# Kernel optimization log

Measured on AMD Instinct MI355X. Metric: run time of the kernel, lower is better.

The kernel has to match this reference:

```python
import jax, jax.numpy as jnp
import numpy as np

BN_EPS = 1e-5


def three_nn(unknown, known):
    # squared pairwise distances via gemm form: ||u||^2 + ||k||^2 - 2 u.k
    # unknown: (B, n, 3), known: (B, m, 3) -> d: (B, n, m)
    u2 = jnp.sum(unknown * unknown, axis=-1, keepdims=True)          # (B, n, 1)
    k2 = jnp.sum(known * known, axis=-1)[:, None, :]                 # (B, 1, m)
    d = u2 + k2 - 2.0 * jnp.einsum('bnc,bmc->bnm', unknown, known)   # (B, n, m)
    neg_d, idx = jax.lax.top_k(-d, 3)                                # 3 smallest
    return -neg_d, idx                                               # (B,n,3), (B,n,3) int32


def three_interpolate(known_feats, idx, weight):
    # known_feats: (B, C, m), idx/weight: (B, n, 3) -> (B, C, n)
    g = jnp.take_along_axis(known_feats[:, :, None, :], idx[:, None, :, :], axis=3)  # (B,C,n,3)
    return jnp.sum(g * weight[:, None, :, :], axis=3)


def conv1x1(x, W, b):
    # x: (B, C_in, N), W: (C_out, C_in), b: (C_out,)
    return jnp.einsum('oc,bcn->bon', W, x) + b[None, :, None]


def batchnorm(x, gamma, beta):
    # training-mode BN over (B, N) per channel, biased variance
    mean = jnp.mean(x, axis=(0, 2), keepdims=True)
    var = jnp.mean((x - mean) ** 2, axis=(0, 2), keepdims=True)
    xn = (x - mean) * jax.lax.rsqrt(var + BN_EPS)
    return xn * gamma[None, :, None] + beta[None, :, None]


def setup_inputs() -> dict:
    key = jax.random.key(0)
    ks = jax.random.split(key, 16)
    B, n, m = 16, 4096, 1024
    C1, C2, C = 128, 256, 256  # in_channels, known feat channels (=mlp[0]), mlp width
    inp = {
        'unknown': jax.random.normal(ks[0], (B, n, 3), jnp.float32),
        'known': jax.random.normal(ks[1], (B, m, 3), jnp.float32),
        'unknow_feats': jax.random.normal(ks[2], (B, C1, n), jnp.float32),
        'known_feats': jax.random.normal(ks[3], (B, C2, m), jnp.float32),
        # mlp_unknow: Conv1d(C1->C) + BN (no relu)
        'Wu': jax.random.normal(ks[4], (C, C1), jnp.float32) * (1.0 / np.sqrt(C1)),
        'bu': jnp.zeros((C,), jnp.float32),
        'gu': jnp.ones((C,), jnp.float32),
        'betau': jnp.zeros((C,), jnp.float32),
        # mlp_convs[0]: Conv1d(C->C) + BN + relu
        'W1': jax.random.normal(ks[5], (C, C), jnp.float32) * (1.0 / np.sqrt(C)),
        'b1': jnp.zeros((C,), jnp.float32),
        'g1': jnp.ones((C,), jnp.float32),
        'beta1': jnp.zeros((C,), jnp.float32),
        # mlp_convs[1]: Conv1d(C->C) + BN + relu
        'W2': jax.random.normal(ks[6], (C, C), jnp.float32) * (1.0 / np.sqrt(C)),
        'b2': jnp.zeros((C,), jnp.float32),
        'g2': jnp.ones((C,), jnp.float32),
        'beta2': jnp.zeros((C,), jnp.float32),
    }
    return inp


def reference(unknown, known, unknow_feats, known_feats,
              Wu, bu, gu, betau, W1, b1, g1, beta1, W2, b2, g2, beta2):
    dist, idx = three_nn(unknown, known)            # squared dists (B,n,3)
    dist_recip = 1.0 / (dist + 1e-8)
    norm = jnp.sum(dist_recip, axis=2, keepdims=True)
    weight = dist_recip / norm
    interpolated = three_interpolate(known_feats, idx, weight)   # (B, 256, n)

    skip = batchnorm(conv1x1(unknow_feats, Wu, bu), gu, betau)   # (B, 256, n)
    x = interpolated + skip
    x = jax.nn.relu(batchnorm(conv1x1(x, W1, b1), g1, beta1))
    x = jax.nn.relu(batchnorm(conv1x1(x, W2, b2), g2, beta2))
    return x
```

## Files before the change

kernel.cpp:

```cpp
#include <hip/hip_runtime.h>
#include <hip/hip_bf16.h>
#include <cstddef>
#include <cstdint>

#define BATCH 16
#define NPTS  4096
#define MPTS  1024
#define PTOT  65536
#define C1    128
#define C2    256

typedef short bf16x8 __attribute__((ext_vector_type(8)));
typedef float f32x4  __attribute__((ext_vector_type(4)));
typedef unsigned int u32x4 __attribute__((ext_vector_type(4)));

static __device__ __forceinline__ float bf2f(unsigned int u16) {
    union { unsigned int i; float f; } v; v.i = u16 << 16; return v.f;
}
static __device__ __forceinline__ unsigned short f2bf(float f) {
    union { float f; unsigned int i; } v; v.f = f;
    unsigned int u = v.i;
    return (unsigned short)((u + 0x7FFFu + ((u >> 16) & 1u)) >> 16);
}

static __device__ __forceinline__ void st_wt_b128(void* p, u32x4 v) {
    asm volatile("global_store_dwordx4 %0, %1, off sc0 sc1" :: "v"(p), "v"(v) : "memory");
}
static __device__ __forceinline__ void st_wt_f128(void* p, f32x4 v) {
    asm volatile("global_store_dwordx4 %0, %1, off sc0 sc1" :: "v"(p), "v"(v) : "memory");
}
static __device__ __forceinline__ void st_wt_b32(void* p, unsigned v) {
    asm volatile("global_store_dword %0, %1, off sc0 sc1" :: "v"(p), "v"(v) : "memory");
}
static __device__ __forceinline__ void st_wt_b16(void* p, unsigned v) {
    asm volatile("global_store_short %0, %1, off sc0 sc1" :: "v"(p), "v"(v) : "memory");
}

template <int SWZ>
__global__ void k_transpose(const float* __restrict__ in, unsigned short* __restrict__ out,
                            int C, int N) {
    __shared__ float tile[64][65];
    int b  = blockIdx.z;
    int n0 = blockIdx.x * 64;
    int c0 = blockIdx.y * 64;
    const float* src = in + (size_t)b * C * N;
    unsigned short* dst = out + (size_t)b * N * C;
    int t  = threadIdx.x;
    int t4 = t >> 6;
    int tn = t & 63;
#pragma unroll
    for (int i = 0; i < 16; ++i) {
        int cc = i * 4 + t4;
        tile[cc][tn] = src[(size_t)(c0 + cc) * N + n0 + tn];
    }
    __syncthreads();
#pragma unroll
    for (int i = 0; i < 16; ++i) {
        int nn = i * 4 + t4;
        int p  = n0 + nn;
        int c  = c0 + tn;
        size_t off;
        if (SWZ) off = (size_t)p * C + (size_t)((((c >> 3) ^ (p & 7)) << 3) + (c & 7));
        else     off = (size_t)p * C + c;
        st_wt_b16(dst + off, (unsigned)f2bf(tile[tn][nn]));
    }
}

__global__ void k_cvt_pack(const float* __restrict__ in, unsigned short* __restrict__ out, int K) {
    int tid = blockIdx.x * 256 + threadIdx.x;
    if (tid >= 256 * K) return;
    int ch = tid / K, k = tid % K;
    int ks = k >> 5, lhi = (k >> 3) & 3, e = k & 7;
    int wv = ch >> 6, i = (ch >> 4) & 3, llo = ch & 15;
    int lane = lhi * 16 + llo;
    st_wt_b16(out + ((size_t)((ks * 16 + wv * 4 + i) * 64 + lane)) * 8 + e,
              (unsigned)f2bf(in[tid]));
}

static __device__ __forceinline__ bool nn_less(float da, int ia, float db, int ib) {
    return (da < db) || (da == db && ia < ib);
}

__global__ void k_three_nn(const float* __restrict__ unknown, const float* __restrict__ known,
                           int* __restrict__ idx_out, float* __restrict__ w_out) {
    __shared__ float4 kpt[MPTS + 4];
    int t  = threadIdx.x;
    int p0 = blockIdx.x * 64;
    int b  = p0 >> 12;
    const float* kb = known + (size_t)b * MPTS * 3;
    for (int i = t; i < MPTS; i += 256) {
        float x = kb[i * 3 + 0], y = kb[i * 3 + 1], z = kb[i * 3 + 2];
        float dd = __fadd_rn(__fadd_rn(__fmul_rn(x, x), __fmul_rn(y, y)), __fmul_rn(z, z));
        float4 v; v.x = x; v.y = y; v.z = z; v.w = dd;
        kpt[i + (i >> 8)] = v;
    }
    __syncthreads();

    int q = t & 3;
    int p = p0 + (t >> 2);
    const float* up = unknown + (size_t)p * 3;
    float ux = up[0], uy = up[1], uz = up[2];
    float u2 = __fadd_rn(__fadd_rn(__fmul_rn(ux, ux), __fmul_rn(uy, uy)), __fmul_rn(uz, uz));

    float d0 = INFINITY, d1 = INFINITY, d2 = INFINITY;
    int   i0 = 0, i1 = 0, i2 = 0;
    int base = q * 257;
#pragma unroll 4
    for (int it = 0; it < 256; ++it) {
        float4 kp = kpt[base + it];
        float dot = __fadd_rn(__fadd_rn(__fmul_rn(ux, kp.x), __fmul_rn(uy, kp.y)),
                              __fmul_rn(uz, kp.z));
        float d = __fsub_rn(__fadd_rn(u2, kp.w), __fmul_rn(2.0f, dot));
        int k = q * 256 + it;
        if (d < d0)      { d2 = d1; i2 = i1; d1 = d0; i1 = i0; d0 = d; i0 = k; }
        else if (d < d1) { d2 = d1; i2 = i1; d1 = d;  i1 = k; }
        else if (d < d2) { d2 = d;  i2 = k; }
    }

#pragma unroll
    for (int m = 1; m <= 2; m <<= 1) {
        float e0 = __shfl_xor(d0, m, 64), e1 = __shfl_xor(d1, m, 64), e2 = __shfl_xor(d2, m, 64);
        int   j0 = __shfl_xor(i0, m, 64), j1 = __shfl_xor(i1, m, 64), j2 = __shfl_xor(i2, m, 64);
        float a0 = d0, a1 = d1, a2 = d2; int x0 = i0, x1 = i1, x2 = i2;
        float b0 = e0, b1 = e1, b2 = e2; int y0 = j0, y1 = j1, y2 = j2;
        bool tk = nn_less(a0, x0, b0, y0);
        d0 = tk ? a0 : b0; i0 = tk ? x0 : y0;
        float na0 = tk ? a1 : a0; int nx0 = tk ? x1 : x0;
        float na1 = tk ? a2 : a1; int nx1 = tk ? x2 : x1;
        float nb0 = tk ? b0 : b1; int ny0 = tk ? y0 : y1;
        float nb1 = tk ? b1 : b2; int ny1 = tk ? y1 : y2;
        tk = nn_less(na0, nx0, nb0, ny0);
        d1 = tk ? na0 : nb0; i1 = tk ? nx0 : ny0;
        float ma0 = tk ? na1 : na0; int mx0 = tk ? nx1 : nx0;
        float mb0 = tk ? nb0 : nb1; int my0 = tk ? ny0 : ny1;
        tk = nn_less(ma0, mx0, mb0, my0);
        d2 = tk ? ma0 : mb0; i2 = tk ? mx0 : my0;
    }

    if (q == 0) {
        float r0 = 1.0f / (d0 + 1e-8f), r1 = 1.0f / (d1 + 1e-8f), r2 = 1.0f / (d2 + 1e-8f);
        float norm = r0 + r1 + r2;
        size_t pg = (size_t)p;
        st_wt_b32(idx_out + pg * 3 + 0, (unsigned)i0);
        st_wt_b32(idx_out + pg * 3 + 1, (unsigned)i1);
        st_wt_b32(idx_out + pg * 3 + 2, (unsigned)i2);
        union { float f; unsigned u; } w0v, w1v, w2v;
        w0v.f = r0 / norm; w1v.f = r1 / norm; w2v.f = r2 / norm;
        st_wt_b32(w_out + pg * 3 + 0, w0v.u);
        st_wt_b32(w_out + pg * 3 + 1, w1v.u);
        st_wt_b32(w_out + pg * 3 + 2, w2v.u);
    }
}

template <int K, int MODE>
__global__ void k_gemm(
        const unsigned short* __restrict__ Wp,
        const unsigned short* __restrict__ X,
        const float* __restrict__ Xf,
        const float* __restrict__ bias,
        const float* __restrict__ aff_a,
        const float* __restrict__ aff_c,
        unsigned short* __restrict__ Y,
        float* __restrict__ partial) {
    constexpr int NK = K / 32;
    constexpr int TILE_BYTES = 64 * K * 2;
    constexpr int SMEM_BYTES = TILE_BYTES > 32768 ? TILE_BYTES : 32768;
    __shared__ char smem[SMEM_BYTES];

    const int t    = threadIdx.x;
    const int p0   = blockIdx.x * 64;
    const int wv   = t >> 6;
    const int lane = t & 63;
    const int lhi  = lane >> 4, llo = lane & 15;

    if (MODE == 0) {
        const char* src = (const char*)(X + (size_t)p0 * K);
        constexpr int ITERS = TILE_BYTES / (256 * 16);
#pragma unroll
        for (int i = 0; i < ITERS; ++i) {
            int off = (i * 256 + t) * 16;
            __builtin_amdgcn_global_load_lds(
                (const __attribute__((address_space(1))) unsigned int*)(src + off),
                (__attribute__((address_space(3))) unsigned int*)(smem + off),
                16, 0, 0);
        }
    } else if (MODE == 1) {
        constexpr int CPR = K / 8;
#pragma unroll
        for (int i = 0; i < (64 * CPR) / 256; ++i) {
            int f   = i * 256 + t;
            int row = f / CPR, qp = f % CPR;
            int col = qp ^ (row & 7);
            uint4 v = *(const uint4*)(X + (size_t)(p0 + row) * K + qp * 8);
            unsigned int w[4] = {v.x, v.y, v.z, v.w};
            float4 a0 = *(const float4*)(aff_a + col * 8);
            float4 a1 = *(const float4*)(aff_a + col * 8 + 4);
            float4 cc0 = *(const float4*)(aff_c + col * 8);
            float4 cc1 = *(const float4*)(aff_c + col * 8 + 4);
            float aa[8] = {a0.x, a0.y, a0.z, a0.w, a1.x, a1.y, a1.z, a1.w};
            float cc[8] = {cc0.x, cc0.y, cc0.z, cc0.w, cc1.x, cc1.y, cc1.z, cc1.w};
#pragma unroll
            for (int q2 = 0; q2 < 4; ++q2) {
                float lo = fmaxf(bf2f(w[q2] & 0xffff) * aa[q2 * 2]     + cc[q2 * 2],     0.0f);
                float hi = fmaxf(bf2f(w[q2] >> 16)    * aa[q2 * 2 + 1] + cc[q2 * 2 + 1], 0.0f);
                w[q2] = (unsigned int)f2bf(lo) | ((unsigned int)f2bf(hi) << 16);
            }
            uint4 o; o.x = w[0]; o.y = w[1]; o.z = w[2]; o.w = w[3];
            *(uint4*)(smem + row * (K * 2) + qp * 16) = o;
        }
    } else {
        int c  = t >> 1;
        int ph = (t & 1) * 32;
        int b  = p0 >> 12;
        const float* src = Xf + ((size_t)b * C1 + c) * NPTS + (p0 & 4095) + ph;
#pragma unroll
        for (int k = 0; k < 8; ++k) {
            float4 v = *(const float4*)(src + k * 4);
#pragma unroll
            for (int e = 0; e < 4; ++e) {
                int p = ph + k * 4 + e;
                float f = (e == 0) ? v.x : (e == 1) ? v.y : (e == 2) ? v.z : v.w;
                *(unsigned short*)(smem + p * (K * 2) + ((((c >> 3) ^ (p & 7)) << 4) + (c & 7) * 2))
                    = f2bf(f);
            }
        }
    }

    const unsigned short* wbase = Wp + ((size_t)(wv * 256) + lane) * 8;
    bf16x8 wA[4], wB[4];
#pragma unroll
    for (int i = 0; i < 4; ++i)
        wA[i] = *(const bf16x8*)(wbase + i * 512);

    __syncthreads();

    f32x4 acc[4][4];
#pragma unroll
    for (int i = 0; i < 4; ++i)
#pragma unroll
        for (int j = 0; j < 4; ++j) acc[i][j] = (f32x4){0.f, 0.f, 0.f, 0.f};

#pragma unroll
    for (int ks = 0; ks < NK; ks += 2) {
#pragma unroll
        for (int i = 0; i < 4; ++i)
            wB[i] = *(const bf16x8*)(wbase + (size_t)(ks + 1) * 8192 + i * 512);
        {
            bf16x8 bb[4];
#pragma unroll
            for (int j = 0; j < 4; ++j) {
                int row = j * 16 + llo;
                int cp  = (ks * 4 + lhi) ^ (row & 7);
                bb[j] = *(const bf16x8*)(smem + row * (K * 2) + cp * 16);
            }
#pragma unroll
            for (int i = 0; i < 4; ++i)
#pragma unroll
                for (int j = 0; j < 4; ++j)
                    acc[i][j] = __builtin_amdgcn_mfma_f32_16x16x32_bf16(wA[i], bb[j], acc[i][j], 0, 0, 0);
        }
        if (ks + 2 < NK) {
#pragma unroll
            for (int i = 0; i < 4; ++i)
                wA[i] = *(const bf16x8*)(wbase + (size_t)(ks + 2) * 8192 + i * 512);
        }
        {
            bf16x8 bb[4];
#pragma unroll
            for (int j = 0; j < 4; ++j) {
                int row = j * 16 + llo;
                int cp  = ((ks + 1) * 4 + lhi) ^ (row & 7);
                bb[j] = *(const bf16x8*)(smem + row * (K * 2) + cp * 16);
            }
#pragma unroll
            for (int i = 0; i < 4; ++i)
#pragma unroll
                for (int j = 0; j < 4; ++j)
                    acc[i][j] = __builtin_amdgcn_mfma_f32_16x16x32_bf16(wB[i], bb[j], acc[i][j], 0, 0, 0);
        }
    }

    __syncthreads();
#pragma unroll
    for (int i = 0; i < 4; ++i) {
        int cbase = wv * 64 + i * 16 + lhi * 4;
        float4 bv = *(const float4*)(bias + cbase);
        int c8 = cbase >> 3, hf = lhi & 1;
        float s0 = 0.f, s1 = 0.f, s2 = 0.f, s3 = 0.f;
        float q0 = 0.f, q1 = 0.f, q2 = 0.f, q3 = 0.f;
#pragma unroll
        for (int j = 0; j < 4; ++j) {
            int row = j * 16 + llo;
            float y0 = acc[i][j][0] + bv.x;
            float y1 = acc[i][j][1] + bv.y;
            float y2 = acc[i][j][2] + bv.z;
            float y3 = acc[i][j][3] + bv.w;
            s0 += y0; q0 += y0 * y0;  s1 += y1; q1 += y1 * y1;
            s2 += y2; q2 += y2 * y2;  s3 += y3; q3 += y3 * y3;
            unsigned int lo = (unsigned int)f2bf(y0) | ((unsigned int)f2bf(y1) << 16);
            unsigned int hi = (unsigned int)f2bf(y2) | ((unsigned int)f2bf(y3) << 16);
            uint2 o; o.x = lo; o.y = hi;
            *(uint2*)(smem + row * 512 + ((c8 ^ (row & 7)) << 4) + hf * 8) = o;
        }
#pragma unroll
        for (int m = 1; m <= 8; m <<= 1) {
            s0 += __shfl_xor(s0, m, 64); q0 += __shfl_xor(q0, m, 64);
            s1 += __shfl_xor(s1, m, 64); q1 += __shfl_xor(q1, m, 64);
            s2 += __shfl_xor(s2, m, 64); q2 += __shfl_xor(q2, m, 64);
            s3 += __shfl_xor(s3, m, 64); q3 += __shfl_xor(q3, m, 64);
        }
        if (llo == 0) {
            f32x4 sv = {s0, s1, s2, s3};
            f32x4 qv = {q0, q1, q2, q3};
            st_wt_f128(partial + (size_t)blockIdx.x * 512 + cbase, sv);
            st_wt_f128(partial + (size_t)blockIdx.x * 512 + 256 + cbase, qv);
        }
    }
    __syncthreads();
    {
        const char* ysrc = smem + wv * 8192 + lane * 16;
        char* ydst = (char*)(Y + (size_t)p0 * 256) + wv * 8192 + lane * 16;
#pragma unroll
        for (int i2 = 0; i2 < 8; ++i2) {
            u32x4 v = *(const u32x4*)(ysrc + i2 * 1024);
            st_wt_b128(ydst + i2 * 1024, v);
        }
    }
}

__global__ void k_red1(const float* __restrict__ partial, float* __restrict__ partA) {
    int t = threadIdx.x, g = blockIdx.x;
    float s = 0.f, q = 0.f;
#pragma unroll
    for (int i = 0; i < 16; ++i) {
        const float* pp = partial + (size_t)(g * 16 + i) * 512;
        s += pp[t]; q += pp[256 + t];
    }
    union { float f; unsigned u; } sv, qv; sv.f = s; qv.f = q;
    st_wt_b32(partA + g * 512 + t, sv.u);
    st_wt_b32(partA + g * 512 + 256 + t, qv.u);
}

__global__ void k_finalize(const float* __restrict__ partA, const float* __restrict__ gamma,
                           const float* __restrict__ beta, float* __restrict__ aff_a,
                           float* __restrict__ aff_c) {
    int c = threadIdx.x;
    float s = 0.f, q = 0.f;
#pragma unroll 8
    for (int i = 0; i < 64; ++i) { s += partA[i * 512 + c]; q += partA[i * 512 + 256 + c]; }
    float mean = s * (1.0f / PTOT);
    float var  = fmaxf(q * (1.0f / PTOT) - mean * mean, 0.0f);
    float a    = gamma[c] / sqrtf(var + 1e-5f);
    union { float f; unsigned u; } av, cv;
    av.f = a; cv.f = beta[c] - mean * a;
    st_wt_b32(aff_a + c, av.u);
    st_wt_b32(aff_c + c, cv.u);
}

__global__ void k_build_x(const unsigned short* __restrict__ y0, const unsigned short* __restrict__ kfT,
                          const int* __restrict__ idx, const float* __restrict__ wgt,
                          const float* __restrict__ aff_a, const float* __restrict__ aff_c,
                          unsigned short* __restrict__ X) {
    int t   = threadIdx.x;
    int p   = blockIdx.x * 8 + (t >> 5);
    int col = t & 31;
    int c0  = col * 8;
    int b   = p >> 12;
    int pos = col ^ (p & 7);
    int i0 = idx[p * 3 + 0], i1 = idx[p * 3 + 1], i2 = idx[p * 3 + 2];
    float w0 = wgt[p * 3 + 0], w1 = wgt[p * 3 + 1], w2 = wgt[p * 3 + 2];
    const size_t kb = (size_t)b * MPTS * C2;
    uint4 v0 = *(const uint4*)(kfT + kb + (size_t)i0 * C2 + c0);
    uint4 v1 = *(const uint4*)(kfT + kb + (size_t)i1 * C2 + c0);
    uint4 v2 = *(const uint4*)(kfT + kb + (size_t)i2 * C2 + c0);
    uint4 vy = *(const uint4*)(y0 + (size_t)p * C2 + pos * 8);
    const unsigned int* u0 = (const unsigned int*)&v0;
    const unsigned int* u1 = (const unsigned int*)&v1;
    const unsigned int* u2 = (const unsigned int*)&v2;
    const unsigned int* uy = (const unsigned int*)&vy;
    unsigned int r[4];
#pragma unroll
    for (int q = 0; q < 4; ++q) {
        int c = c0 + q * 2;
        float lo = w0 * bf2f(u0[q] & 0xffff) + w1 * bf2f(u1[q] & 0xffff) + w2 * bf2f(u2[q] & 0xffff)
                 + bf2f(uy[q] & 0xffff) * aff_a[c] + aff_c[c];
        float hi = w0 * bf2f(u0[q] >> 16) + w1 * bf2f(u1[q] >> 16) + w2 * bf2f(u2[q] >> 16)
                 + bf2f(uy[q] >> 16) * aff_a[c + 1] + aff_c[c + 1];
        r[q] = (unsigned int)f2bf(lo) | ((unsigned int)f2bf(hi) << 16);
    }
    u32x4 vout; vout.x = r[0]; vout.y = r[1]; vout.z = r[2]; vout.w = r[3];
    st_wt_b128(X + (size_t)p * C2 + pos * 8, vout);
}

__global__ void k_final(const unsigned short* __restrict__ Y2, const float* __restrict__ aff_a,
                        const float* __restrict__ aff_c, float* __restrict__ out) {
    __shared__ float tile[64][65];
    int p0 = blockIdx.x * 64;
    int c0 = blockIdx.y * 64;
    int t  = threadIdx.x;
    int t4 = t >> 6, t64 = t & 63;
#pragma unroll
    for (int i = 0; i < 16; ++i) {
        int r = i * 4 + t4;
        int p = p0 + r;
        int c = c0 + t64;
        float v = bf2f(Y2[(size_t)p * 256 + (((c >> 3) ^ (p & 7)) << 3) + (c & 7)])
                  * aff_a[c] + aff_c[c];
        tile[t64][r] = fmaxf(v, 0.0f);
    }
    __syncthreads();
    int b   = p0 >> 12;
    int pin = p0 & 4095;
#pragma unroll
    for (int i = 0; i < 16; ++i) {
        int cc = i * 4 + t4;
        __builtin_nontemporal_store(tile[cc][t64],
            out + ((size_t)b * 256 + c0 + cc) * 4096 + pin + t64);
    }
}

extern "C" void kernel_launch(void* const* d_in, const int* in_sizes, int n_in,
                              void* d_out, int out_size, void* d_ws, size_t ws_size,
                              hipStream_t stream) {
    const float* unknown = (const float*)d_in[0];
    const float* known   = (const float*)d_in[1];
    const float* ufeat   = (const float*)d_in[2];
    const float* kfeat   = (const float*)d_in[3];
    const float* Wu      = (const float*)d_in[4];
    const float* bu      = (const float*)d_in[5];
    const float* gu      = (const float*)d_in[6];
    const float* betau   = (const float*)d_in[7];
    const float* W1      = (const float*)d_in[8];
    const float* b1      = (const float*)d_in[9];
    const float* g1      = (const float*)d_in[10];
    const float* beta1   = (const float*)d_in[11];
    const float* W2      = (const float*)d_in[12];
    const float* b2      = (const float*)d_in[13];
    const float* g2      = (const float*)d_in[14];
    const float* beta2   = (const float*)d_in[15];
    float* out = (float*)d_out;

    char* ws = (char*)d_ws;
    unsigned short* reg0 = (unsigned short*)ws;
    unsigned short* ybuf = (unsigned short*)(ws + ((size_t)32 << 20));
    unsigned short* kfT  = (unsigned short*)(ws + ((size_t)64 << 20));
    unsigned short* Wub  = (unsigned short*)(ws + ((size_t)72 << 20));
    unsigned short* W1b  = Wub + 256 * 128;
    unsigned short* W2b  = W1b + 256 * 256;
    int*   idxb = (int*)(W2b + 256 * 256);
    float* wgtb = (float*)(idxb + (size_t)PTOT * 3);
    float* affa0 = wgtb + (size_t)PTOT * 3;
    float* affc0 = affa0 + 256;
    float* affa1 = affc0 + 256;
    float* affc1 = affa1 + 256;
    float* affa2 = affc1 + 256;
    float* affc2 = affa2 + 256;
    float* part0  = (float*)(ws + ((size_t)16 << 20));
    float* partA0 = (float*)(ws + ((size_t)18 << 20));
    float* part12  = (float*)(ws + ((size_t)64 << 20));
    float* partA12 = (float*)(ws + ((size_t)66 << 20));
    if (ws_size < ((size_t)75 << 20)) return;

    k_transpose<0><<<dim3(MPTS / 64, C2 / 64, BATCH), 256, 0, stream>>>(kfeat, kfT, C2, MPTS);
    k_cvt_pack<<<128, 256, 0, stream>>>(Wu, Wub, 128);
    k_cvt_pack<<<256, 256, 0, stream>>>(W1, W1b, 256);
    k_cvt_pack<<<256, 256, 0, stream>>>(W2, W2b, 256);

    k_three_nn<<<PTOT / 64, 256, 0, stream>>>(unknown, known, idxb, wgtb);

    k_gemm<C1, 2><<<PTOT / 64, 256, 0, stream>>>(Wub, nullptr, ufeat, bu, nullptr, nullptr,
                                                 ybuf, part0);
    k_red1<<<64, 256, 0, stream>>>(part0, partA0);
    k_finalize<<<1, 256, 0, stream>>>(partA0, gu, betau, affa0, affc0);

    k_build_x<<<PTOT / 8, 256, 0, stream>>>(ybuf, kfT, idxb, wgtb, affa0, affc0, reg0);

    k_gemm<C2, 0><<<PTOT / 64, 256, 0, stream>>>(W1b, reg0, nullptr, b1, nullptr, nullptr,
                                                 ybuf, part12);
    k_red1<<<64, 256, 0, stream>>>(part12, partA12);
    k_finalize<<<1, 256, 0, stream>>>(partA12, g1, beta1, affa1, affc1);

    k_gemm<C2, 1><<<PTOT / 64, 256, 0, stream>>>(W2b, ybuf, nullptr, b2, affa1, affc1,
                                                 reg0, part12);
    k_red1<<<64, 256, 0, stream>>>(part12, partA12);
    k_finalize<<<1, 256, 0, stream>>>(partA12, g2, beta2, affa2, affc2);

    k_final<<<dim3(PTOT / 64, 4), 256, 0, stream>>>(reg0, affa2, affc2, out);

    (void)in_sizes; (void)n_in; (void)out_size;
}
```

Before: 201.5 us.

## Process two 64-point tiles per GEMM block and store outputs directly

Each GEMM block now loads two 64-point activation tiles into a doubled LDS buffer and computes them one after the other, halving the grid size. The LDS-staged write-back of Y is replaced by direct 8-byte global stores in swizzled layout, and the write-through store in build_x becomes a plain store. The aims are to cut launch/block overhead and the extra LDS round trip, at the cost of more LDS per block (lower occupancy), fewer blocks to spread across CUs, and narrower, less coalesced output stores.

```diff
diff --git a/kernel.cpp b/kernel.cpp
--- a/kernel.cpp
+++ b/kernel.cpp
@@ -23,9 +23,6 @@
     return (unsigned short)((u + 0x7FFFu + ((u >> 16) & 1u)) >> 16);
 }
 
-static __device__ __forceinline__ void st_wt_b128(void* p, u32x4 v) {
-    asm volatile("global_store_dwordx4 %0, %1, off sc0 sc1" :: "v"(p), "v"(v) : "memory");
-}
 static __device__ __forceinline__ void st_wt_f128(void* p, f32x4 v) {
     asm volatile("global_store_dwordx4 %0, %1, off sc0 sc1" :: "v"(p), "v"(v) : "memory");
 }
@@ -163,167 +160,167 @@
         unsigned short* __restrict__ Y,
         float* __restrict__ partial) {
     constexpr int NK = K / 32;
-    constexpr int TILE_BYTES = 64 * K * 2;
-    constexpr int SMEM_BYTES = TILE_BYTES > 32768 ? TILE_BYTES : 32768;
-    __shared__ char smem[SMEM_BYTES];
+    constexpr int TB = 64 * K * 2;
+    __shared__ char smem[2 * TB];
 
     const int t    = threadIdx.x;
-    const int p0   = blockIdx.x * 64;
+    const int p0   = blockIdx.x * 128;
     const int wv   = t >> 6;
     const int lane = t & 63;
     const int lhi  = lane >> 4, llo = lane & 15;
 
-    if (MODE == 0) {
-        const char* src = (const char*)(X + (size_t)p0 * K);
-        constexpr int ITERS = TILE_BYTES / (256 * 16);
-#pragma unroll
-        for (int i = 0; i < ITERS; ++i) {
-            int off = (i * 256 + t) * 16;
-            __builtin_amdgcn_global_load_lds(
-                (const __attribute__((address_space(1))) unsigned int*)(src + off),
-                (__attribute__((address_space(3))) unsigned int*)(smem + off),
-                16, 0, 0);
+#pragma unroll
+    for (int h = 0; h < 2; ++h) {
+        char* dsts = smem + h * TB;
+        if (MODE == 0) {
+            const char* src = (const char*)(X + (size_t)(p0 + 64 * h) * K);
+            constexpr int ITERS = TB / (256 * 16);
+#pragma unroll
+            for (int i = 0; i < ITERS; ++i) {
+                int off = (i * 256 + t) * 16;
+                __builtin_amdgcn_global_load_lds(
+                    (const __attribute__((address_space(1))) unsigned int*)(src + off),
+                    (__attribute__((address_space(3))) unsigned int*)(dsts + off),
+                    16, 0, 0);
+            }
+        } else if (MODE == 1) {
+            constexpr int CPR = K / 8;
+#pragma unroll
+            for (int i = 0; i < (64 * CPR) / 256; ++i) {
+                int f   = i * 256 + t;
+                int row = f / CPR, qp = f % CPR;
+                int col = qp ^ (row & 7);
+                uint4 v = *(const uint4*)(X + (size_t)(p0 + 64 * h + row) * K + qp * 8);
+                unsigned int w[4] = {v.x, v.y, v.z, v.w};
+                float4 a0 = *(const float4*)(aff_a + col * 8);
+                float4 a1 = *(const float4*)(aff_a + col * 8 + 4);
+                float4 cc0 = *(const float4*)(aff_c + col * 8);
+                float4 cc1 = *(const float4*)(aff_c + col * 8 + 4);
+                float aa[8] = {a0.x, a0.y, a0.z, a0.w, a1.x, a1.y, a1.z, a1.w};
+                float cc[8] = {cc0.x, cc0.y, cc0.z, cc0.w, cc1.x, cc1.y, cc1.z, cc1.w};
+#pragma unroll
+                for (int q2 = 0; q2 < 4; ++q2) {
+                    float lo = fmaxf(bf2f(w[q2] & 0xffff) * aa[q2 * 2]     + cc[q2 * 2],     0.0f);
+                    float hi = fmaxf(bf2f(w[q2] >> 16)    * aa[q2 * 2 + 1] + cc[q2 * 2 + 1], 0.0f);
+                    w[q2] = (unsigned int)f2bf(lo) | ((unsigned int)f2bf(hi) << 16);
+                }
+                uint4 o; o.x = w[0]; o.y = w[1]; o.z = w[2]; o.w = w[3];
+                *(uint4*)(dsts + row * (K * 2) + qp * 16) = o;
+            }
+        } else {
+            int c  = t >> 1;
+            int ph = (t & 1) * 32;
+            int tp = p0 + 64 * h;
+            int b  = tp >> 12;
+            const float* src = Xf + ((size_t)b * C1 + c) * NPTS + (tp & 4095) + ph;
+#pragma unroll
+            for (int k = 0; k < 8; ++k) {
+                float4 v = *(const float4*)(src + k * 4);
+#pragma unroll
+                for (int e = 0; e < 4; ++e) {
+                    int p = ph + k * 4 + e;
+                    float f = (e == 0) ? v.x : (e == 1) ? v.y : (e == 2) ? v.z : v.w;
+                    *(unsigned short*)(dsts + p * (K * 2) +
+                                       ((((c >> 3) ^ (p & 7)) << 4) + (c & 7) * 2)) = f2bf(f);
+                }
+            }
         }
-    } else if (MODE == 1) {
-        constexpr int CPR = K / 8;
-#pragma unroll
-        for (int i = 0; i < (64 * CPR) / 256; ++i) {
-            int f   = i * 256 + t;
-            int row = f / CPR, qp = f % CPR;
-            int col = qp ^ (row & 7);
-            uint4 v = *(const uint4*)(X + (size_t)(p0 + row) * K + qp * 8);
-            unsigned int w[4] = {v.x, v.y, v.z, v.w};
-            float4 a0 = *(const float4*)(aff_a + col * 8);
-            float4 a1 = *(const float4*)(aff_a + col * 8 + 4);
-            float4 cc0 = *(const float4*)(aff_c + col * 8);
-            float4 cc1 = *(const float4*)(aff_c + col * 8 + 4);
-            float aa[8] = {a0.x, a0.y, a0.z, a0.w, a1.x, a1.y, a1.z, a1.w};
-            float cc[8] = {cc0.x, cc0.y, cc0.z, cc0.w, cc1.x, cc1.y, cc1.z, cc1.w};
-#pragma unroll
-            for (int q2 = 0; q2 < 4; ++q2) {
-                float lo = fmaxf(bf2f(w[q2] & 0xffff) * aa[q2 * 2]     + cc[q2 * 2],     0.0f);
-                float hi = fmaxf(bf2f(w[q2] >> 16)    * aa[q2 * 2 + 1] + cc[q2 * 2 + 1], 0.0f);
-                w[q2] = (unsigned int)f2bf(lo) | ((unsigned int)f2bf(hi) << 16);
-            }
-            uint4 o; o.x = w[0]; o.y = w[1]; o.z = w[2]; o.w = w[3];
-            *(uint4*)(smem + row * (K * 2) + qp * 16) = o;
+    }
+
+    __syncthreads();
+
+    const unsigned short* wbase = Wp + ((size_t)(wv * 256) + lane) * 8;
+
+#pragma unroll
+    for (int tt = 0; tt < 2; ++tt) {
+        const char* sm = smem + tt * TB;
+        const int tp0 = p0 + 64 * tt;
+
+        bf16x8 wA[4], wB[4];
+#pragma unroll
+        for (int i = 0; i < 4; ++i)
+            wA[i] = *(const bf16x8*)(wbase + i * 512);
+
+        f32x4 acc[4][4];
+#pragma unroll
+        for (int i = 0; i < 4; ++i)
+#pragma unroll
+            for (int j = 0; j < 4; ++j) acc[i][j] = (f32x4){0.f, 0.f, 0.f, 0.f};
+
+#pragma unroll
+        for (int ks = 0; ks < NK; ks += 2) {
+#pragma unroll
+            for (int i = 0; i < 4; ++i)
+                wB[i] = *(const bf16x8*)(wbase + (size_t)(ks + 1) * 8192 + i * 512);
+            {
+                bf16x8 bb[4];
+#pragma unroll
+                for (int j = 0; j < 4; ++j) {
+                    int row = j * 16 + llo;
+                    int cp  = (ks * 4 + lhi) ^ (row & 7);
+                    bb[j] = *(const bf16x8*)(sm + row * (K * 2) + cp * 16);
+                }
+#pragma unroll
+                for (int i = 0; i < 4; ++i)
+#pragma unroll
+                    for (int j = 0; j < 4; ++j)
+                        acc[i][j] = __builtin_amdgcn_mfma_f32_16x16x32_bf16(wA[i], bb[j], acc[i][j], 0, 0, 0);
+            }
+            if (ks + 2 < NK) {
+#pragma unroll
+                for (int i = 0; i < 4; ++i)
+                    wA[i] = *(const bf16x8*)(wbase + (size_t)(ks + 2) * 8192 + i * 512);
+            }
+            {
+                bf16x8 bb[4];
+#pragma unroll
+                for (int j = 0; j < 4; ++j) {
+                    int row = j * 16 + llo;
+                    int cp  = ((ks + 1) * 4 + lhi) ^ (row & 7);
+                    bb[j] = *(const bf16x8*)(sm + row * (K * 2) + cp * 16);
+                }
+#pragma unroll
+                for (int i = 0; i < 4; ++i)
+#pragma unroll
+                    for (int j = 0; j < 4; ++j)
+                        acc[i][j] = __builtin_amdgcn_mfma_f32_16x16x32_bf16(wB[i], bb[j], acc[i][j], 0, 0, 0);
+            }
         }
-    } else {
-        int c  = t >> 1;
-        int ph = (t & 1) * 32;
-        int b  = p0 >> 12;
-        const float* src = Xf + ((size_t)b * C1 + c) * NPTS + (p0 & 4095) + ph;
-#pragma unroll
-        for (int k = 0; k < 8; ++k) {
-            float4 v = *(const float4*)(src + k * 4);
-#pragma unroll
-            for (int e = 0; e < 4; ++e) {
-                int p = ph + k * 4 + e;
-                float f = (e == 0) ? v.x : (e == 1) ? v.y : (e == 2) ? v.z : v.w;
-                *(unsigned short*)(smem + p * (K * 2) + ((((c >> 3) ^ (p & 7)) << 4) + (c & 7) * 2))
-                    = f2bf(f);
-            }
-        }
-    }
-
-    const unsigned short* wbase = Wp + ((size_t)(wv * 256) + lane) * 8;
-    bf16x8 wA[4], wB[4];
-#pragma unroll
-    for (int i = 0; i < 4; ++i)
-        wA[i] = *(const bf16x8*)(wbase + i * 512);
-
-    __syncthreads();
-
-    f32x4 acc[4][4];
-#pragma unroll
-    for (int i = 0; i < 4; ++i)
-#pragma unroll
-        for (int j = 0; j < 4; ++j) acc[i][j] = (f32x4){0.f, 0.f, 0.f, 0.f};
-
-#pragma unroll
-    for (int ks = 0; ks < NK; ks += 2) {
-#pragma unroll
-        for (int i = 0; i < 4; ++i)
-            wB[i] = *(const bf16x8*)(wbase + (size_t)(ks + 1) * 8192 + i * 512);
-        {
-            bf16x8 bb[4];
+
+#pragma unroll
+        for (int i = 0; i < 4; ++i) {
+            int cbase = wv * 64 + i * 16 + lhi * 4;
+            float4 bv = *(const float4*)(bias + cbase);
+            int c8 = cbase >> 3, hf = lhi & 1;
+            float s0 = 0.f, s1 = 0.f, s2 = 0.f, s3 = 0.f;
+            float q0 = 0.f, q1 = 0.f, q2 = 0.f, q3 = 0.f;
 #pragma unroll
             for (int j = 0; j < 4; ++j) {
-                int row = j * 16 + llo;
-                int cp  = (ks * 4 + lhi) ^ (row & 7);
-                bb[j] = *(const bf16x8*)(smem + row * (K * 2) + cp * 16);
-            }
-#pragma unroll
-            for (int i = 0; i < 4; ++i)
-#pragma unroll
-                for (int j = 0; j < 4; ++j)
-                    acc[i][j] = __builtin_amdgcn_mfma_f32_16x16x32_bf16(wA[i], bb[j], acc[i][j], 0, 0, 0);
-        }
-        if (ks + 2 < NK) {
-#pragma unroll
-            for (int i = 0; i < 4; ++i)
-                wA[i] = *(const bf16x8*)(wbase + (size_t)(ks + 2) * 8192 + i * 512);
-        }
-        {
-            bf16x8 bb[4];
-#pragma unroll
-            for (int j = 0; j < 4; ++j) {
-                int row = j * 16 + llo;
-                int cp  = ((ks + 1) * 4 + lhi) ^ (row & 7);
-                bb[j] = *(const bf16x8*)(smem + row * (K * 2) + cp * 16);
-            }
-#pragma unroll
-            for (int i = 0; i < 4; ++i)
-#pragma unroll
-                for (int j = 0; j < 4; ++j)
-                    acc[i][j] = __builtin_amdgcn_mfma_f32_16x16x32_bf16(wB[i], bb[j], acc[i][j], 0, 0, 0);
-        }
-    }
-
-    __syncthreads();
-#pragma unroll
-    for (int i = 0; i < 4; ++i) {
-        int cbase = wv * 64 + i * 16 + lhi * 4;
-        float4 bv = *(const float4*)(bias + cbase);
-        int c8 = cbase >> 3, hf = lhi & 1;
-        float s0 = 0.f, s1 = 0.f, s2 = 0.f, s3 = 0.f;
-        float q0 = 0.f, q1 = 0.f, q2 = 0.f, q3 = 0.f;
-#pragma unroll
-        for (int j = 0; j < 4; ++j) {
-            int row = j * 16 + llo;
-            float y0 = acc[i][j][0] + bv.x;
-            float y1 = acc[i][j][1] + bv.y;
-            float y2 = acc[i][j][2] + bv.z;
-            float y3 = acc[i][j][3] + bv.w;
-            s0 += y0; q0 += y0 * y0;  s1 += y1; q1 += y1 * y1;
-            s2 += y2; q2 += y2 * y2;  s3 += y3; q3 += y3 * y3;
-            unsigned int lo = (unsigned int)f2bf(y0) | ((unsigned int)f2bf(y1) << 16);
-            unsigned int hi = (unsigned int)f2bf(y2) | ((unsigned int)f2bf(y3) << 16);
-            uint2 o; o.x = lo; o.y = hi;
-            *(uint2*)(smem + row * 512 + ((c8 ^ (row & 7)) << 4) + hf * 8) = o;
-        }
-#pragma unroll
-        for (int m = 1; m <= 8; m <<= 1) {
-            s0 += __shfl_xor(s0, m, 64); q0 += __shfl_xor(q0, m, 64);
-            s1 += __shfl_xor(s1, m, 64); q1 += __shfl_xor(q1, m, 64);
-            s2 += __shfl_xor(s2, m, 64); q2 += __shfl_xor(q2, m, 64);
-            s3 += __shfl_xor(s3, m, 64); q3 += __shfl_xor(q3, m, 64);
-        }
-        if (llo == 0) {
-            f32x4 sv = {s0, s1, s2, s3};
-            f32x4 qv = {q0, q1, q2, q3};
-            st_wt_f128(partial + (size_t)blockIdx.x * 512 + cbase, sv);
-            st_wt_f128(partial + (size_t)blockIdx.x * 512 + 256 + cbase, qv);
-        }
-    }
-    __syncthreads();
-    {
-        const char* ysrc = smem + wv * 8192 + lane * 16;
-        char* ydst = (char*)(Y + (size_t)p0 * 256) + wv * 8192 + lane * 16;
-#pragma unroll
-        for (int i2 = 0; i2 < 8; ++i2) {
-            u32x4 v = *(const u32x4*)(ysrc + i2 * 1024);
-            st_wt_b128(ydst + i2 * 1024, v);
+                int p = tp0 + j * 16 + llo;
+                float y0 = acc[i][j][0] + bv.x;
+                float y1 = acc[i][j][1] + bv.y;
+                float y2 = acc[i][j][2] + bv.z;
+                float y3 = acc[i][j][3] + bv.w;
+                s0 += y0; q0 += y0 * y0;  s1 += y1; q1 += y1 * y1;
+                s2 += y2; q2 += y2 * y2;  s3 += y3; q3 += y3 * y3;
+                unsigned int lo = (unsigned int)f2bf(y0) | ((unsigned int)f2bf(y1) << 16);
+                unsigned int hi = (unsigned int)f2bf(y2) | ((unsigned int)f2bf(y3) << 16);
+                uint2 o; o.x = lo; o.y = hi;
+                *(uint2*)(Y + (size_t)p * 256 + ((c8 ^ (p & 7)) << 3) + hf * 4) = o;
+            }
+#pragma unroll
+            for (int m = 1; m <= 8; m <<= 1) {
+                s0 += __shfl_xor(s0, m, 64); q0 += __shfl_xor(q0, m, 64);
+                s1 += __shfl_xor(s1, m, 64); q1 += __shfl_xor(q1, m, 64);
+                s2 += __shfl_xor(s2, m, 64); q2 += __shfl_xor(q2, m, 64);
+                s3 += __shfl_xor(s3, m, 64); q3 += __shfl_xor(q3, m, 64);
+            }
+            if (llo == 0) {
+                f32x4 sv = {s0, s1, s2, s3};
+                f32x4 qv = {q0, q1, q2, q3};
+                st_wt_f128(partial + (size_t)(2 * blockIdx.x + tt) * 512 + cbase, sv);
+                st_wt_f128(partial + (size_t)(2 * blockIdx.x + tt) * 512 + 256 + cbase, qv);
+            }
         }
     }
 }
@@ -388,8 +385,8 @@
                  + bf2f(uy[q] >> 16) * aff_a[c + 1] + aff_c[c + 1];
         r[q] = (unsigned int)f2bf(lo) | ((unsigned int)f2bf(hi) << 16);
     }
-    u32x4 vout; vout.x = r[0]; vout.y = r[1]; vout.z = r[2]; vout.w = r[3];
-    st_wt_b128(X + (size_t)p * C2 + pos * 8, vout);
+    uint4 vout; vout.x = r[0]; vout.y = r[1]; vout.z = r[2]; vout.w = r[3];
+    *(uint4*)(X + (size_t)p * C2 + pos * 8) = vout;
 }
 
 __global__ void k_final(const unsigned short* __restrict__ Y2, const float* __restrict__ aff_a,
@@ -468,20 +465,20 @@
 
     k_three_nn<<<PTOT / 64, 256, 0, stream>>>(unknown, known, idxb, wgtb);
 
-    k_gemm<C1, 2><<<PTOT / 64, 256, 0, stream>>>(Wub, nullptr, ufeat, bu, nullptr, nullptr,
-                                                 ybuf, part0);
+    k_gemm<C1, 2><<<PTOT / 128, 256, 0, stream>>>(Wub, nullptr, ufeat, bu, nullptr, nullptr,
+                                                  ybuf, part0);
     k_red1<<<64, 256, 0, stream>>>(part0, partA0);
     k_finalize<<<1, 256, 0, stream>>>(partA0, gu, betau, affa0, affc0);
 
     k_build_x<<<PTOT / 8, 256, 0, stream>>>(ybuf, kfT, idxb, wgtb, affa0, affc0, reg0);
 
-    k_gemm<C2, 0><<<PTOT / 64, 256, 0, stream>>>(W1b, reg0, nullptr, b1, nullptr, nullptr,
-                                                 ybuf, part12);
+    k_gemm<C2, 0><<<PTOT / 128, 256, 0, stream>>>(W1b, reg0, nullptr, b1, nullptr, nullptr,
+                                                  ybuf, part12);
     k_red1<<<64, 256, 0, stream>>>(part12, partA12);
     k_finalize<<<1, 256, 0, stream>>>(partA12, g1, beta1, affa1, affc1);
 
-    k_gemm<C2, 1><<<PTOT / 64, 256, 0, stream>>>(W2b, ybuf, nullptr, b2, affa1, affc1,
-                                                 reg0, part12);
+    k_gemm<C2, 1><<<PTOT / 128, 256, 0, stream>>>(W2b, ybuf, nullptr, b2, affa1, affc1,
+                                                  reg0, part12);
     k_red1<<<64, 256, 0, stream>>>(part12, partA12);
     k_finalize<<<1, 256, 0, stream>>>(partA12, g2, beta2, affa2, affc2);
 
```

After: 251.2 us. 1.25x slower.
